# Kernel tuning notes

Measured on AMD Instinct MI355X. Metric: run time of the kernel, lower is better.

Reference implementation:

```python
import jax, jax.numpy as jnp
import numpy as np

BS, S, H, T = 16, 256, 1024, 32  # batch, num entities, hidden, num relation tags
N_TAGS = 7


def setup_inputs() -> dict:
    key = jax.random.key(0)
    k0, k1, k2, k3 = jax.random.split(key, 4)
    seq_embedding = jax.random.normal(k0, (BS, H), dtype=jnp.float32)
    entities_embeddings = jax.random.normal(k1, (BS, S, H), dtype=jnp.float32)
    entities_tags = jax.random.randint(k2, (BS, S), 0, N_TAGS)
    # relation_classifier: Linear(3*H -> T)
    W = jax.random.normal(k3, (T, 3 * H), dtype=jnp.float32) * 0.02
    b = jnp.zeros((T,), dtype=jnp.float32)
    return {
        "seq_embedding": seq_embedding,
        "entities_embeddings": entities_embeddings,
        "W": W,
        "b": b,
        "entities_tags": entities_tags,
    }


def reference(seq_embedding, entities_embeddings, W, b, entities_tags):
    # Original (eval mode, dropout=identity):
    #   pred[b,i,j] = W @ concat(E[b,i], E[b,j], S[b]) + bias
    # (arg1/arg2/all_seq linears and tag embeddings are dead code in the
    #  original forward: their outputs are never used.)
    # Decompose W = [W1 | W2 | W3] along the feature axis; mathematically
    # identical to materializing the (bs,S,S,3H) concat tensor.
    h = entities_embeddings.shape[-1]
    W1, W2, W3 = W[:, :h], W[:, h:2 * h], W[:, 2 * h:]
    p1 = jnp.einsum('bih,th->bit', entities_embeddings, W1)  # arg1 contribution
    p2 = jnp.einsum('bjh,th->bjt', entities_embeddings, W2)  # arg2 contribution
    ps = seq_embedding @ W3.T + b                             # seq + bias
    # (bs, S, S, T)
    return p1[:, :, None, :] + p2[:, None, :, :] + ps[:, None, None, :]
```

## Files before the change

### kernel.cpp

```cpp
#include <hip/hip_runtime.h>

#define BS 16
#define S  256
#define H  1024
#define T  32

#define PS_OFF 0
#define P1_OFF 512
#define P2_OFF (P1_OFF + BS * S * T)

typedef __bf16 bf16x8 __attribute__((ext_vector_type(8)));
typedef float  f32x4  __attribute__((ext_vector_type(4)));
typedef float  f4n    __attribute__((ext_vector_type(4)));

__device__ inline bf16x8 to_bf8(float4 lo, float4 hi) {
    bf16x8 r;
    r[0] = (__bf16)lo.x; r[1] = (__bf16)lo.y; r[2] = (__bf16)lo.z; r[3] = (__bf16)lo.w;
    r[4] = (__bf16)hi.x; r[5] = (__bf16)hi.y; r[6] = (__bf16)hi.z; r[7] = (__bf16)hi.w;
    return r;
}

__global__ __launch_bounds__(1024) void gemm_ps(
    const float* __restrict__ seq, const float* __restrict__ E,
    const float* __restrict__ W, const float* __restrict__ bias,
    float* __restrict__ ws)
{
    const int tid = threadIdx.x;
    const int lane = tid & 63, wv = tid >> 6;

    if (blockIdx.x < 32) {
        float* ps = ws + PS_OFF;
        const int o = blockIdx.x * 16 + wv;
        const int bb = o >> 5, t = o & 31;
        const float4* sp = (const float4*)(seq + (size_t)bb * H) + lane * 4;
        const float4* wp = (const float4*)(W + (size_t)t * (3 * H) + 2 * H) + lane * 4;
        float acc = 0.f;
        #pragma unroll
        for (int k = 0; k < 4; ++k) {
            float4 a = sp[k], w = wp[k];
            acc += a.x * w.x + a.y * w.y + a.z * w.z + a.w * w.w;
        }
        #pragma unroll
        for (int m = 32; m >= 1; m >>= 1) acc += __shfl_xor(acc, m);
        if (lane == 0) ps[o] = acc + bias[t];
        return;
    }

    __shared__ __align__(16) __bf16 Ebf[16][1032];
    __shared__ __align__(16) float  pacc[4][16][64];

    const int m0 = (blockIdx.x - 32) * 16;
    const int ks = wv >> 2;
    const int cg = wv & 3;
    const int kbeg = ks * 256;

    const int col = cg * 16 + (lane & 15);
    const int ksub = (lane >> 4) * 8;
    const float* wbase = W + (size_t)(col & 31) * (3 * H)
                           + ((col >= 32) ? H : 0) + kbeg + ksub;
    bf16x8 bfrag[8];
    #pragma unroll
    for (int s = 0; s < 8; ++s)
        bfrag[s] = to_bf8(*(const float4*)(wbase + s * 32),
                          *(const float4*)(wbase + s * 32 + 4));

    #pragma unroll
    for (int i = 0; i < 2; ++i) {
        int c = tid + i * 1024;
        int row = c >> 7, c8 = c & 127;
        const float4* src = (const float4*)(E + (size_t)(m0 + row) * H + c8 * 8);
        *(bf16x8*)&Ebf[row][c8 * 8] = to_bf8(src[0], src[1]);
    }
    __syncthreads();

    f32x4 acc = {0.f, 0.f, 0.f, 0.f};
    const int erow = lane & 15;
    const int kof = kbeg + ksub;
    #pragma unroll
    for (int s = 0; s < 8; ++s) {
        bf16x8 a = *(const bf16x8*)&Ebf[erow][kof + s * 32];
        acc = __builtin_amdgcn_mfma_f32_16x16x32_bf16(a, bfrag[s], acc, 0, 0, 0);
    }

    const int orow = (lane >> 4) * 4;
    #pragma unroll
    for (int r = 0; r < 4; ++r)
        pacc[ks][orow + r][col] = acc[r];
    __syncthreads();

    {
        const int row = tid >> 6, c = tid & 63;
        float v = (pacc[0][row][c] + pacc[1][row][c])
                + (pacc[2][row][c] + pacc[3][row][c]);
        if (c < 32) (ws + P1_OFF)[(size_t)(m0 + row) * T + c] = v;
        else        (ws + P2_OFF)[(size_t)(m0 + row) * T + (c - 32)] = v;
    }
}

__global__ __launch_bounds__(256) void bcast_add(
    const float* __restrict__ ws, float* __restrict__ out)
{
    const int blk = blockIdx.x;
    const int b = blk >> 8, i = blk & 255;
    const int tid = threadIdx.x;

    const float4 s1v = *(const float4*)((ws + P1_OFF)
                       + (size_t)(b * S + i) * T + (tid & 7) * 4);
    const float4 psv = *(const float4*)((ws + PS_OFF) + b * T + (tid & 7) * 4);
    float4 s;
    s.x = s1v.x + psv.x; s.y = s1v.y + psv.y;
    s.z = s1v.z + psv.z; s.w = s1v.w + psv.w;

    const float4* p2v = (const float4*)(ws + P2_OFF) + (size_t)b * (S * T / 4);
    float4* ov = (float4*)out + (size_t)(b * S + i) * (S * T / 4);

    #pragma unroll
    for (int k = tid; k < S * T / 4; k += 256) {
        float4 v = p2v[k];
        f4n r;
        r.x = v.x + s.x; r.y = v.y + s.y; r.z = v.z + s.z; r.w = v.w + s.w;
        __builtin_nontemporal_store(r, (f4n*)&ov[k]);
    }
}

extern "C" void kernel_launch(void* const* d_in, const int* in_sizes, int n_in,
                              void* d_out, int out_size, void* d_ws, size_t ws_size,
                              hipStream_t stream)
{
    const float* seq  = (const float*)d_in[0];
    const float* E    = (const float*)d_in[1];
    const float* W    = (const float*)d_in[2];
    const float* bias = (const float*)d_in[3];
    float* out = (float*)d_out;
    float* ws  = (float*)d_ws;

    gemm_ps<<<288, 1024, 0, stream>>>(seq, E, W, bias, ws);
    bcast_add<<<BS * S, 256, 0, stream>>>(ws, out);
}
```

Baseline: 40.68 us.

## Halve GEMM block size, prefetch E loads early, use plain output stores

Reworks the GEMM kernel to use 512-thread blocks where each wave covers a 512-wide K chunk with 16 MFMA steps. The E tile global loads are issued before the W fragment loads so their latencies overlap. The seq-projection part is split across 64 smaller blocks, and the split-K reduction now uses two partial buffers. The broadcast kernel replaces nontemporal stores with ordinary stores, which changes cache behaviour for the large output write.

```diff
diff --git a/kernel.cpp b/kernel.cpp
--- a/kernel.cpp
+++ b/kernel.cpp
@@ -11,7 +11,6 @@
 
 typedef __bf16 bf16x8 __attribute__((ext_vector_type(8)));
 typedef float  f32x4  __attribute__((ext_vector_type(4)));
-typedef float  f4n    __attribute__((ext_vector_type(4)));
 
 __device__ inline bf16x8 to_bf8(float4 lo, float4 hi) {
     bf16x8 r;
@@ -20,7 +19,7 @@
     return r;
 }
 
-__global__ __launch_bounds__(1024) void gemm_ps(
+__global__ __launch_bounds__(512) void gemm_ps(
     const float* __restrict__ seq, const float* __restrict__ E,
     const float* __restrict__ W, const float* __restrict__ bias,
     float* __restrict__ ws)
@@ -28,9 +27,9 @@
     const int tid = threadIdx.x;
     const int lane = tid & 63, wv = tid >> 6;
 
-    if (blockIdx.x < 32) {
+    if (blockIdx.x < 64) {
         float* ps = ws + PS_OFF;
-        const int o = blockIdx.x * 16 + wv;
+        const int o = blockIdx.x * 8 + wv;
         const int bb = o >> 5, t = o & 31;
         const float4* sp = (const float4*)(seq + (size_t)bb * H) + lane * 4;
         const float4* wp = (const float4*)(W + (size_t)t * (3 * H) + 2 * H) + lane * 4;
@@ -47,51 +46,58 @@
     }
 
     __shared__ __align__(16) __bf16 Ebf[16][1032];
-    __shared__ __align__(16) float  pacc[4][16][64];
+    __shared__ __align__(16) float  pacc[2][16][64];
 
-    const int m0 = (blockIdx.x - 32) * 16;
-    const int ks = wv >> 2;
+    const int m0 = (blockIdx.x - 64) * 16;
+    const int kc = wv >> 2;
     const int cg = wv & 3;
-    const int kbeg = ks * 256;
+    const int kbeg = kc * 512;
+
+    float4 tmpa[4], tmpb[4];
+    #pragma unroll
+    for (int i = 0; i < 4; ++i) {
+        int c = tid + i * 512;
+        int row = c >> 7, c8 = c & 127;
+        const float4* src = (const float4*)(E + (size_t)(m0 + row) * H + c8 * 8);
+        tmpa[i] = src[0]; tmpb[i] = src[1];
+    }
 
     const int col = cg * 16 + (lane & 15);
     const int ksub = (lane >> 4) * 8;
     const float* wbase = W + (size_t)(col & 31) * (3 * H)
                            + ((col >= 32) ? H : 0) + kbeg + ksub;
-    bf16x8 bfrag[8];
+    bf16x8 bfrag[16];
     #pragma unroll
-    for (int s = 0; s < 8; ++s)
+    for (int s = 0; s < 16; ++s)
         bfrag[s] = to_bf8(*(const float4*)(wbase + s * 32),
                           *(const float4*)(wbase + s * 32 + 4));
 
     #pragma unroll
-    for (int i = 0; i < 2; ++i) {
-        int c = tid + i * 1024;
+    for (int i = 0; i < 4; ++i) {
+        int c = tid + i * 512;
         int row = c >> 7, c8 = c & 127;
-        const float4* src = (const float4*)(E + (size_t)(m0 + row) * H + c8 * 8);
-        *(bf16x8*)&Ebf[row][c8 * 8] = to_bf8(src[0], src[1]);
+        *(bf16x8*)&Ebf[row][c8 * 8] = to_bf8(tmpa[i], tmpb[i]);
     }
     __syncthreads();
 
     f32x4 acc = {0.f, 0.f, 0.f, 0.f};
     const int erow = lane & 15;
-    const int kof = kbeg + ksub;
     #pragma unroll
-    for (int s = 0; s < 8; ++s) {
-        bf16x8 a = *(const bf16x8*)&Ebf[erow][kof + s * 32];
+    for (int s = 0; s < 16; ++s) {
+        bf16x8 a = *(const bf16x8*)&Ebf[erow][kbeg + s * 32 + ksub];
         acc = __builtin_amdgcn_mfma_f32_16x16x32_bf16(a, bfrag[s], acc, 0, 0, 0);
     }
 
     const int orow = (lane >> 4) * 4;
     #pragma unroll
     for (int r = 0; r < 4; ++r)
-        pacc[ks][orow + r][col] = acc[r];
+        pacc[kc][orow + r][col] = acc[r];
     __syncthreads();
 
-    {
-        const int row = tid >> 6, c = tid & 63;
-        float v = (pacc[0][row][c] + pacc[1][row][c])
-                + (pacc[2][row][c] + pacc[3][row][c]);
+    #pragma unroll
+    for (int e = tid; e < 1024; e += 512) {
+        const int row = e >> 6, c = e & 63;
+        float v = pacc[0][row][c] + pacc[1][row][c];
         if (c < 32) (ws + P1_OFF)[(size_t)(m0 + row) * T + c] = v;
         else        (ws + P2_OFF)[(size_t)(m0 + row) * T + (c - 32)] = v;
     }
@@ -117,9 +123,9 @@
     #pragma unroll
     for (int k = tid; k < S * T / 4; k += 256) {
         float4 v = p2v[k];
-        f4n r;
+        float4 r;
         r.x = v.x + s.x; r.y = v.y + s.y; r.z = v.z + s.z; r.w = v.w + s.w;
-        __builtin_nontemporal_store(r, (f4n*)&ov[k]);
+        ov[k] = r;
     }
 }
 
@@ -134,6 +140,6 @@
     float* out = (float*)d_out;
     float* ws  = (float*)d_ws;
 
-    gemm_ps<<<288, 1024, 0, stream>>>(seq, E, W, bias, ws);
+    gemm_ps<<<320, 512, 0, stream>>>(seq, E, W, bias, ws);
     bcast_add<<<BS * S, 256, 0, stream>>>(ws, out);
 }
```

After: 37.93 us. -6.7%, faster.
